# Optimization experiments

Hardware: AMD Instinct MI355X
Metric: run time of the kernel (lower is better)

The kernel has to match this reference:

```python
import jax, jax.numpy as jnp
import numpy as np

B, L, E, H = 8, 2048, 1024, 16
D = E // H
EPS = 1e-6


def setup_inputs() -> dict:
    key = jax.random.key(0)
    ks = jax.random.split(key, 9)
    s = 1.0 / np.sqrt(E)
    def lin_w(k):
        return jax.random.uniform(k, (E, E), jnp.float32, -s, s)
    def lin_b(k):
        return jax.random.uniform(k, (E,), jnp.float32, -s, s)
    return {
        "query": jax.random.normal(ks[0], (B, L, E), jnp.float32),
        "Wq": lin_w(ks[1]), "bq": lin_b(ks[2]),
        "Wk": lin_w(ks[3]), "bk": lin_b(ks[4]),
        "Wv": lin_w(ks[5]), "bv": lin_b(ks[6]),
        "Wo": lin_w(ks[7]), "bo": lin_b(ks[8]),
    }


def reference(query, Wq, bq, Wk, bk, Wv, bv, Wo, bo):
    bsz, tgt_len, embed_dim = query.shape
    n_head = H
    head_dim = embed_dim // n_head
    m = tgt_len  # src_len == tgt_len (self-attention)

    # projections (torch Linear with W stored as (in, out) here)
    q = query @ Wq + bq
    k = query @ Wk + bk
    v = query @ Wv + bv

    # (B, L, E) -> (B, H, L, D), softmax feature map over head dim
    def to_heads(x):
        return x.reshape(bsz, tgt_len, n_head, head_dim).transpose(0, 2, 1, 3)

    q = jax.nn.softmax(to_heads(q), axis=-1)
    k = jax.nn.softmax(to_heads(k), axis=-1)
    v = to_heads(v)
    comp_q = 1.0 - q
    comp_k = 1.0 - k

    # cosFormer positional reweighting: idx = (pi/2) * (1..m) / m
    idx = (np.pi / 2) * jnp.arange(1, m + 1, dtype=jnp.float32) / m  # (L,)
    sin = jnp.sin(idx)[None, None, :, None]  # (1,1,L,1)
    cos = jnp.cos(idx)[None, None, :, None]

    def feat(x):  # (B,H,L,D) -> (B,H,L,2D)
        return jnp.concatenate([x * sin, x * cos], axis=-1)

    qf, comp_qf = feat(q), feat(comp_q)
    kf, comp_kf = feat(k), feat(comp_k)

    def branch(qf_, kf_):
        kv = jnp.einsum('bhld,bhlm->bhdm', kf_, v)            # (B,H,2D,D)
        z = 1.0 / jnp.maximum(
            jnp.einsum('bhld,bhd->bhl', qf_, kf_.sum(axis=2)), EPS)
        return jnp.einsum('bhld,bhdm,bhl->bhlm', qf_, kv, z)  # (B,H,L,D)

    attn = branch(qf, kf) + branch(comp_qf, comp_kf)

    # torch: (B*H,L,D).transpose(0,1).view(L,B,E)
    out = attn.transpose(2, 0, 1, 3).reshape(tgt_len, bsz, embed_dim)
    out = out @ Wo + bo
    # torch final: .view(bsz, tgt_len, n_feat) -- raw reshape, no transpose
    return out.reshape(bsz, tgt_len, embed_dim)
```

## Files before the change

kernel.cpp:

```cpp
#include <hip/hip_runtime.h>
#include <hip/hip_bf16.h>
#include <cstdint>

#define B_   8
#define L_   2048
#define E_   1024
#define H_   16
#define D_   64
#define M_   (B_ * L_)
#define EPS_ 1e-6f
#define PI2_ 1.57079632679f

typedef __bf16 bf16;
typedef __bf16 bf16x8 __attribute__((ext_vector_type(8)));
typedef __bf16 bf16x4 __attribute__((ext_vector_type(4)));
typedef float  floatx4 __attribute__((ext_vector_type(4)));

__device__ inline void async_cp16(const void* g, void* l) {
  __builtin_amdgcn_global_load_lds(
      (__attribute__((address_space(1))) void*)const_cast<void*>(g),
      (__attribute__((address_space(3))) void*)l,
      16, 0, 0);
}

__global__ __launch_bounds__(256) void k_convert_x(const float* __restrict__ x,
                                                   bf16* __restrict__ o) {
  size_t i = ((size_t)blockIdx.x * 256 + threadIdx.x) * 8;
  floatx4 a = *(const floatx4*)(x + i);
  floatx4 b = *(const floatx4*)(x + i + 4);
  bf16x8 r;
  r[0] = (bf16)a[0]; r[1] = (bf16)a[1]; r[2] = (bf16)a[2]; r[3] = (bf16)a[3];
  r[4] = (bf16)b[0]; r[5] = (bf16)b[1]; r[6] = (bf16)b[2]; r[7] = (bf16)b[3];
  *(bf16x8*)(o + i) = r;
}

struct TArgs { const float* src[4]; bf16* dst[4]; };

__global__ __launch_bounds__(256) void k_transpose_w(TArgs t) {
  __shared__ float tile[32][33];
  const float* src = t.src[blockIdx.z];
  bf16* dst = t.dst[blockIdx.z];
  int bx = blockIdx.x, by = blockIdx.y;
  int x = threadIdx.x, y = threadIdx.y;
#pragma unroll
  for (int i = 0; i < 4; i++) {
    int r = by * 32 + y + i * 8;
    tile[y + i * 8][x] = src[(size_t)r * E_ + bx * 32 + x];
  }
  __syncthreads();
#pragma unroll
  for (int i = 0; i < 4; i++) {
    int r = bx * 32 + y + i * 8;
    dst[(size_t)r * E_ + by * 32 + x] = (bf16)tile[x][y + i * 8];
  }
}

#define BAR()   asm volatile("s_barrier" ::: "memory")
#define LGKM0() asm volatile("s_waitcnt lgkmcnt(0)" ::: "memory")
#define VMW4()  asm volatile("s_waitcnt vmcnt(4)" ::: "memory")
#define VMW0()  asm volatile("s_waitcnt vmcnt(0)" ::: "memory")
#define MFMA_   __builtin_amdgcn_mfma_f32_16x16x32_bf16

#define GEMM_TILE(t_, c_) {                                                    \
    const int t = (t_); const int c = (c_);                                    \
    bf16x8 a0[4][2], a1[4][2], b0[2][2], b1[2][2];                             \
                                                                  \
    _Pragma("unroll") for (int i = 0; i < 4; i++) {                            \
      a0[i][0] = RDA(c, 0, i); a0[i][1] = RDA(c, 1, i); }                      \
    _Pragma("unroll") for (int j = 0; j < 2; j++) {                            \
      b0[j][0] = RDB(c, 0, j); b0[j][1] = RDB(c, 1, j); }                      \
    if (t + 1 < 16) STAGE(c ^ 1, 0, t + 1, 0);                                 \
    BAR(); LGKM0();                                                            \
    __builtin_amdgcn_s_setprio(1);                                             \
    _Pragma("unroll") for (int i = 0; i < 4; i++)                              \
      _Pragma("unroll") for (int j = 0; j < 2; j++) {                          \
        acc[i][j] = MFMA_(a0[i][0], b0[j][0], acc[i][j], 0, 0, 0);             \
        acc[i][j] = MFMA_(a0[i][1], b0[j][1], acc[i][j], 0, 0, 0); }           \
    __builtin_amdgcn_s_setprio(0);                                             \
    BAR();                                                                     \
                                                                  \
    _Pragma("unroll") for (int j = 0; j < 2; j++) {                            \
      b1[j][0] = RDB(c, 0, j + 2); b1[j][1] = RDB(c, 1, j + 2); }              \
    if (t + 1 < 16) STAGE(c ^ 1, 0, t + 1, 1);                                 \
    BAR(); LGKM0();                                                            \
    __builtin_amdgcn_s_setprio(1);                                             \
    _Pragma("unroll") for (int i = 0; i < 4; i++)                              \
      _Pragma("unroll") for (int j = 0; j < 2; j++) {                          \
        acc[i][j + 2] = MFMA_(a0[i][0], b1[j][0], acc[i][j + 2], 0, 0, 0);     \
        acc[i][j + 2] = MFMA_(a0[i][1], b1[j][1], acc[i][j + 2], 0, 0, 0); }   \
    __builtin_amdgcn_s_setprio(0);                                             \
    BAR();                                                                     \
                                                                  \
    _Pragma("unroll") for (int i = 0; i < 4; i++) {                            \
      a1[i][0] = RDA(c, 0, i + 4); a1[i][1] = RDA(c, 1, i + 4); }              \
    if (t + 2 < 16) STAGE(c, 1, t + 2, 0);                                     \
    BAR(); LGKM0();                                                            \
    __builtin_amdgcn_s_setprio(1);                                             \
    _Pragma("unroll") for (int i = 0; i < 4; i++)                              \
      _Pragma("unroll") for (int j = 0; j < 2; j++) {                          \
        acc[i + 4][j + 2] = MFMA_(a1[i][0], b1[j][0], acc[i + 4][j + 2], 0, 0, 0); \
        acc[i + 4][j + 2] = MFMA_(a1[i][1], b1[j][1], acc[i + 4][j + 2], 0, 0, 0); } \
    __builtin_amdgcn_s_setprio(0);                                             \
    BAR();                                                                     \
                                                                  \
    if (t < 14) { STAGE(c, 1, t + 2, 1); VMW4(); } else { VMW0(); }            \
    BAR();                                                                     \
    __builtin_amdgcn_s_setprio(1);                                             \
    _Pragma("unroll") for (int i = 0; i < 4; i++)                              \
      _Pragma("unroll") for (int j = 0; j < 2; j++) {                          \
        acc[i + 4][j] = MFMA_(a1[i][0], b0[j][0], acc[i + 4][j], 0, 0, 0);     \
        acc[i + 4][j] = MFMA_(a1[i][1], b0[j][1], acc[i + 4][j], 0, 0, 0); }   \
    __builtin_amdgcn_s_setprio(0);                                             \
    BAR();                                                                     \
  }

__device__ __forceinline__ void gemm256_core(const bf16* __restrict__ Agl,
                                             const bf16* __restrict__ Bgl,
                                             int bm, int bn, bf16* ldsb,
                                             floatx4 (&acc)[8][4]) {
  const int tid  = threadIdx.x;
  const int wid  = tid >> 6;
  const int lane = tid & 63;
  const int quad = lane >> 4;
  const int l15  = lane & 15;
  const int wm   = wid >> 2;
  const int wn   = wid & 3;
  const int rb   = wn * 32;
  const int gcol = wm * 32 + (((lane & 3) * 8) ^ ((lane & 32) ? 16 : 0));
  const bf16* pA = Agl + (size_t)(bm * 256 + rb + (lane >> 2)) * E_ + gcol;
  const bf16* pB = Bgl + (size_t)(bn * 256 + rb + (lane >> 2)) * E_ + gcol;
  const int aCol = (quad * 8) ^ ((l15 & 8) ? 16 : 0);

  auto LDSP = [&](int c, int mat, int qq, int row, int col) -> bf16* {
    return ldsb + ((((c * 2 + mat) * 2 + qq) * 256 + row) * 32 + col);
  };
  auto STAGE = [&](int c, int mat, int tt, int h) {
    const bf16* g = (mat ? pB : pA) + (size_t)(h * 128) * E_ + tt * 64;
    bf16* lp = LDSP(c, mat, wm, h * 128 + rb, 0);
    async_cp16(g, lp);
    async_cp16(g + (size_t)16 * E_, lp + 16 * 32);
  };
  auto RDA = [&](int c, int qq, int i) -> bf16x8 {
    return *(const bf16x8*)LDSP(c, 0, qq, wm * 128 + i * 16 + l15, aCol);
  };
  auto RDB = [&](int c, int qq, int j) -> bf16x8 {
    return *(const bf16x8*)LDSP(c, 1, qq, wn * 64 + j * 16 + l15, aCol);
  };

  STAGE(0, 1, 0, 0); STAGE(0, 1, 0, 1);
  STAGE(0, 0, 0, 0); STAGE(0, 0, 0, 1);
  STAGE(1, 1, 1, 0); STAGE(1, 1, 1, 1);
  VMW4();
  BAR();

#pragma unroll 1
  for (int tb = 0; tb < 16; tb += 2) {
    GEMM_TILE(tb, 0)
    GEMM_TILE(tb + 1, 1)
  }
}

__global__ __launch_bounds__(512, 2) void k_gemm_qkv256(
    const bf16* __restrict__ A, const bf16* __restrict__ Wt,
    const float* __restrict__ bq, const float* __restrict__ bk,
    const float* __restrict__ bv,
    bf16* __restrict__ QTb, bf16* __restrict__ KTb, bf16* __restrict__ VT) {
  __shared__ __attribute__((aligned(16))) bf16 ldsb[2 * 2 * 2 * 256 * 32];
  const int id  = blockIdx.x;
  const int xcd = id & 7, rr = id >> 3;
  const int bm  = xcd * 8 + rr / 12;
  const int cz  = rr % 12;
  const int bn  = cz & 3, z = cz >> 2;
  const bf16* Bgl = Wt + (size_t)z * E_ * E_;

  floatx4 acc[8][4] = {};
  gemm256_core(A, Bgl, bm, bn, ldsb, acc);

  const int tid  = threadIdx.x;
  const int wid  = tid >> 6;
  const int lane = tid & 63;
  const int quad = lane >> 4;
  const int l15  = lane & 15;
  const int wm   = wid >> 2, wn = wid & 3;
  const float* bias = (z == 0) ? bq : (z == 1) ? bk : bv;
  float bb[4];
#pragma unroll
  for (int j = 0; j < 4; j++) bb[j] = bias[bn * 256 + wn * 64 + j * 16 + l15];

  if (z < 2) {
#pragma unroll
    for (int i = 0; i < 8; i++)
#pragma unroll
      for (int r = 0; r < 4; r++) {
        float v0 = acc[i][0][r] + bb[0];
        float v1 = acc[i][1][r] + bb[1];
        float v2 = acc[i][2][r] + bb[2];
        float v3 = acc[i][3][r] + bb[3];
        float m = fmaxf(fmaxf(v0, v1), fmaxf(v2, v3));
        m = fmaxf(m, __shfl_xor(m, 1));
        m = fmaxf(m, __shfl_xor(m, 2));
        m = fmaxf(m, __shfl_xor(m, 4));
        m = fmaxf(m, __shfl_xor(m, 8));
        v0 = __expf(v0 - m); v1 = __expf(v1 - m);
        v2 = __expf(v2 - m); v3 = __expf(v3 - m);
        float s = v0 + v1 + v2 + v3;
        s += __shfl_xor(s, 1); s += __shfl_xor(s, 2);
        s += __shfl_xor(s, 4); s += __shfl_xor(s, 8);
        const float inv = 1.f / s;
        acc[i][0][r] = v0 * inv; acc[i][1][r] = v1 * inv;
        acc[i][2][r] = v2 * inv; acc[i][3][r] = v3 * inv;
      }
  } else {
#pragma unroll
    for (int i = 0; i < 8; i++)
#pragma unroll
      for (int j = 0; j < 4; j++) {
        acc[i][j][0] += bb[j]; acc[i][j][1] += bb[j];
        acc[i][j][2] += bb[j]; acc[i][j][3] += bb[j];
      }
  }

  bf16* OT = (z == 0) ? QTb : (z == 1) ? KTb : VT;
#pragma unroll
  for (int i = 0; i < 8; i++)
#pragma unroll
    for (int j = 0; j < 4; j++) {
      const int c  = bn * 256 + wn * 64 + j * 16 + l15;
      const int r0 = bm * 256 + wm * 128 + i * 16 + quad * 4;
      const int h = c >> 6, d = c & 63;
      const int b = r0 >> 11, l = r0 & 2047;
      bf16x4 rv;
      rv[0] = (bf16)acc[i][j][0]; rv[1] = (bf16)acc[i][j][1];
      rv[2] = (bf16)acc[i][j][2]; rv[3] = (bf16)acc[i][j][3];
      *(bf16x4*)&OT[(((size_t)(b * 16 + h) * 64 + d) * 2048) + l] = rv;
    }
}

__global__ __launch_bounds__(512, 2) void k_gemm_final256(
    const bf16* __restrict__ A, const bf16* __restrict__ Bt,
    const float* __restrict__ bias, float* __restrict__ C) {
  __shared__ __attribute__((aligned(16))) bf16 ldsb[2 * 2 * 2 * 256 * 32];
  const int id  = blockIdx.x;
  const int xcd = id & 7, rr = id >> 3;
  const int bm  = xcd * 8 + (rr >> 2);
  const int bn  = rr & 3;

  floatx4 acc[8][4] = {};
  gemm256_core(A, Bt, bm, bn, ldsb, acc);

  const int tid  = threadIdx.x;
  const int wid  = tid >> 6;
  const int lane = tid & 63;
  const int quad = lane >> 4;
  const int l15  = lane & 15;
  const int wm   = wid >> 2, wn = wid & 3;
#pragma unroll
  for (int i = 0; i < 8; i++)
#pragma unroll
    for (int j = 0; j < 4; j++) {
      const int col = bn * 256 + wn * 64 + j * 16 + l15;
      const float bb = bias[col];
#pragma unroll
      for (int r = 0; r < 4; r++) {
        const int row = bm * 256 + wm * 128 + i * 16 + quad * 4 + r;
        C[(size_t)row * E_ + col] = acc[i][j][r] + bb;
      }
    }
}

__global__ __launch_bounds__(256) void k_kv(const bf16* __restrict__ KTb,
                                            const bf16* __restrict__ VT,
                                            float* __restrict__ kvp) {
  __shared__ __attribute__((aligned(16))) bf16 ktb[64 * 32];
  __shared__ __attribute__((aligned(16))) bf16 vt[64 * 32];
  __shared__ __attribute__((aligned(16))) bf16 Bsn[64 * 40];
  __shared__ __attribute__((aligned(16))) bf16 Bcs[64 * 40];
  __shared__ float snl[32], csl[32];
  const int kseg = blockIdx.x;
  const int bh   = blockIdx.y;
  const int t = threadIdx.x;
  const int wid = t >> 6, lane = t & 63;
  const int quad = lane >> 4, l15 = lane & 15;
  const int wm = wid >> 1, wn = wid & 1;

  const bf16* ktg = KTb + (size_t)bh * 64 * 2048;
  const bf16* vtg = VT  + (size_t)bh * 64 * 2048;

  floatx4 acc[4][2] = {};
  float rs = 0.f;
  const int d_ = t & 63, h_ = t >> 6;

  for (int it = 0; it < 16; it++) {
    const int l0 = kseg * 512 + it * 32;
    {
      const int r = lane >> 2, ch = lane & 3;
      const bf16* gk = ktg + (size_t)(wid * 16 + r) * 2048 + l0 + ((ch ^ (r & 1)) * 8);
      async_cp16(gk, &ktb[(wid * 16) * 32]);
      const bf16* gv = vtg + (size_t)(wid * 16 + r) * 2048 + l0 + ch * 8;
      async_cp16(gv, &vt[(wid * 16) * 32]);
    }
    if (t < 32) {
      const float ang = PI2_ * (float)(l0 + t + 1) / (float)L_;
      snl[t] = __sinf(ang); csl[t] = __cosf(ang);
    }
    __syncthreads();

    {
      const int row = t >> 2, cc = (t & 3) * 8;
      bf16x8 v = *(const bf16x8*)&vt[row * 32 + cc];
      bf16x8 a, b;
#pragma unroll
      for (int e = 0; e < 8; e++) {
        const float f = (float)v[e];
        a[e] = (bf16)(f * snl[cc + e]);
        b[e] = (bf16)(f * csl[cc + e]);
      }
      *(bf16x8*)&Bsn[row * 40 + cc] = a;
      *(bf16x8*)&Bcs[row * 40 + cc] = b;
    }
    if (t < 128) {
      float r8 = 0.f;
#pragma unroll
      for (int p = 0; p < 4; p++) {
        bf16x8 v = *(const bf16x8*)&ktb[d_ * 32 + p * 8];
        const int gl = (p ^ (d_ & 1)) * 8;
#pragma unroll
        for (int e = 0; e < 8; e++)
          r8 += (float)v[e] * (h_ ? csl[gl + e] : snl[gl + e]);
      }
      rs += r8;
    }
    __syncthreads();

    bf16x8 af[4], bfm[2];
    const bf16* Bsel = wm ? Bcs : Bsn;
#pragma unroll
    for (int i = 0; i < 4; i++)
      af[i] = *(const bf16x8*)&ktb[(i * 16 + l15) * 32 + ((quad ^ (l15 & 1)) * 8)];
#pragma unroll
    for (int j = 0; j < 2; j++)
      bfm[j] = *(const bf16x8*)&Bsel[(wn * 32 + j * 16 + l15) * 40 + quad * 8];
#pragma unroll
    for (int i = 0; i < 4; i++)
#pragma unroll
      for (int j = 0; j < 2; j++)
        acc[i][j] = __builtin_amdgcn_mfma_f32_16x16x32_bf16(af[i], bfm[j], acc[i][j], 0, 0, 0);
    __syncthreads();
  }

  float* C = kvp + (size_t)(kseg * 128 + bh) * 128 * 68;
#pragma unroll
  for (int i = 0; i < 4; i++)
#pragma unroll
    for (int j = 0; j < 2; j++) {
      const int col = wn * 32 + j * 16 + l15;
#pragma unroll
      for (int r = 0; r < 4; r++) {
        const int row = wm * 64 + i * 16 + quad * 4 + r;
        C[(size_t)row * 68 + col] = acc[i][j][r];
      }
    }
  if (t < 128) C[(size_t)t * 68 + 64] = rs;
}

__global__ __launch_bounds__(64) void k_consts(const float* __restrict__ kvp,
                                               bf16* __restrict__ KVT,
                                               float* __restrict__ ksbuf) {
  const int bh = blockIdx.x;
  const int dp = threadIdx.x;
  const size_t gs = (size_t)128 * 128 * 68;
  const float* P = kvp + (size_t)bh * 128 * 68;
  bf16* kr = KVT + (size_t)(bh * 64 + dp) * 160;
  float sk0 = 0.f, sk1 = 0.f;
#pragma unroll 8
  for (int f = 0; f < 128; f++) {
    float v = P[(size_t)f * 68 + dp] + P[gs + (size_t)f * 68 + dp]
            + P[2 * gs + (size_t)f * 68 + dp] + P[3 * gs + (size_t)f * 68 + dp];
    kr[f] = (bf16)v;
    if (f < 64) sk0 += v; else sk1 += v;
  }
  float ks0 = P[(size_t)dp * 68 + 64] + P[gs + (size_t)dp * 68 + 64]
            + P[2 * gs + (size_t)dp * 68 + 64] + P[3 * gs + (size_t)dp * 68 + 64];
  float ks1 = P[(size_t)(64 + dp) * 68 + 64] + P[gs + (size_t)(64 + dp) * 68 + 64]
            + P[2 * gs + (size_t)(64 + dp) * 68 + 64] + P[3 * gs + (size_t)(64 + dp) * 68 + 64];
  ksbuf[(size_t)bh * 136 + dp]      = ks0;
  ksbuf[(size_t)bh * 136 + 64 + dp] = ks1;
  float sks0 = ks0, sks1 = ks1;
#pragma unroll
  for (int o = 1; o < 64; o <<= 1) { sks0 += __shfl_xor(sks0, o); sks1 += __shfl_xor(sks1, o); }
  kr[128] = (bf16)(62.f * sk0);
  kr[129] = (bf16)(62.f * sk1);
#pragma unroll
  for (int f = 130; f < 160; f++) kr[f] = (bf16)0.f;
  if (dp == 0) {
    ksbuf[(size_t)bh * 136 + 128] = sks0;
    ksbuf[(size_t)bh * 136 + 129] = sks1;
  }
}

#define ASTR 168
__global__ __launch_bounds__(256) void k_attn(const bf16* __restrict__ QTb,
                                              const bf16* __restrict__ KVT,
                                              const float* __restrict__ ksbuf,
                                              bf16* __restrict__ attn) {
  __shared__ __attribute__((aligned(16))) bf16 Abuf[128 * ASTR];
  __shared__ __attribute__((aligned(16))) bf16 Bbuf[64 * ASTR];
  __shared__ float ksl[136];
  const int lc = blockIdx.x;
  const int bh = blockIdx.y;
  const int b = bh >> 4, h = bh & 15;
  const int t = threadIdx.x;

  {
    const bf16* src = KVT + (size_t)bh * 64 * 160;
#pragma unroll
    for (int i = 0; i < 5; i++) {
      const int idx = t + i * 256;
      const int row = idx / 20, ch = idx % 20;
      *(bf16x8*)&Bbuf[row * ASTR + ch * 8] = *(const bf16x8*)(src + row * 160 + ch * 8);
    }
    if (t < 130) ksl[t] = ksbuf[(size_t)bh * 136 + t];
  }
  __syncthreads();

  if (t < 128) {
    const int l = lc * 128 + t;
    const bf16* qp = QTb + (size_t)bh * 64 * 2048 + l;
    float xv[64];
#pragma unroll
    for (int d = 0; d < 64; d++) xv[d] = (float)qp[(size_t)d * 2048];
    float t0 = 0.f, t1 = 0.f;
#pragma unroll
    for (int d = 0; d < 64; d++) {
      t0 += xv[d] * ksl[d];
      t1 += xv[d] * ksl[64 + d];
    }
    const float SKS0 = ksl[128], SKS1 = ksl[129];
    const float ang = PI2_ * (float)(l + 1) / (float)L_;
    const float sn = __sinf(ang), cs = __cosf(ang);
    const float den1 = sn * t0 + cs * t1;
    const float den2 = sn * (62.f * SKS0 + t0) + cs * (62.f * SKS1 + t1);
    const float z1 = 1.f / fmaxf(den1, EPS_);
    const float z2 = 1.f / fmaxf(den2, EPS_);
    const float zz = z1 + z2;
    const float a0 = zz * sn, a1 = zz * cs;
    bf16* ar = &Abuf[t * ASTR];
#pragma unroll
    for (int g = 0; g < 8; g++) {
      bf16x8 w;
#pragma unroll
      for (int j = 0; j < 8; j++) w[j] = (bf16)(a0 * xv[g * 8 + j]);
      *(bf16x8*)(ar + g * 8) = w;
    }
#pragma unroll
    for (int g = 0; g < 8; g++) {
      bf16x8 w;
#pragma unroll
      for (int j = 0; j < 8; j++) w[j] = (bf16)(a1 * xv[g * 8 + j]);
      *(bf16x8*)(ar + 64 + g * 8) = w;
    }
    bf16x8 wt = {};
    wt[0] = (bf16)(z2 * sn); wt[1] = (bf16)(z2 * cs);
    *(bf16x8*)(ar + 128) = wt;
    bf16x8 zr = {};
    *(bf16x8*)(ar + 136) = zr;
    *(bf16x8*)(ar + 144) = zr;
    *(bf16x8*)(ar + 152) = zr;
  }
  __syncthreads();

  const int wid = t >> 6, lane = t & 63;
  const int quad = lane >> 4, l15 = lane & 15;
  const int wm = wid >> 1, wn = wid & 1;
  floatx4 acc[4][2] = {};
#pragma unroll
  for (int kk = 0; kk < 5; kk++) {
    bf16x8 af[4], bfm[2];
#pragma unroll
    for (int i = 0; i < 4; i++)
      af[i] = *(const bf16x8*)&Abuf[(wm * 64 + i * 16 + l15) * ASTR + kk * 32 + quad * 8];
#pragma unroll
    for (int j = 0; j < 2; j++)
      bfm[j] = *(const bf16x8*)&Bbuf[(wn * 32 + j * 16 + l15) * ASTR + kk * 32 + quad * 8];
#pragma unroll
    for (int i = 0; i < 4; i++)
#pragma unroll
      for (int j = 0; j < 2; j++)
        acc[i][j] = __builtin_amdgcn_mfma_f32_16x16x32_bf16(af[i], bfm[j], acc[i][j], 0, 0, 0);
  }
#pragma unroll
  for (int i = 0; i < 4; i++)
#pragma unroll
    for (int j = 0; j < 2; j++) {
      const int dp = wn * 32 + j * 16 + l15;
#pragma unroll
      for (int r = 0; r < 4; r++) {
        const int l = lc * 128 + wm * 64 + i * 16 + quad * 4 + r;
        attn[((size_t)l * B_ + b) * E_ + h * 64 + dp] = (bf16)acc[i][j][r];
      }
    }
}

extern "C" void kernel_launch(void* const* d_in, const int* in_sizes, int n_in,
                              void* d_out, int out_size, void* d_ws, size_t ws_size,
                              hipStream_t stream) {
  (void)in_sizes; (void)n_in; (void)out_size; (void)ws_size;
  const float* query = (const float*)d_in[0];
  const float* Wq = (const float*)d_in[1];
  const float* bq = (const float*)d_in[2];
  const float* Wk = (const float*)d_in[3];
  const float* bk = (const float*)d_in[4];
  const float* Wv = (const float*)d_in[5];
  const float* bv = (const float*)d_in[6];
  const float* Wo = (const float*)d_in[7];
  const float* bo = (const float*)d_in[8];

  char* ws = (char*)d_ws;
  bf16*  QTb  = (bf16*) (ws + 0);
  bf16*  KTb  = (bf16*) (ws + 33554432);
  bf16*  VT   = (bf16*) (ws + 67108864);
  bf16*  Wt   = (bf16*) (ws + 100663296);
  bf16*  Xbf  = (bf16*) (ws + 109051904);
  bf16*  attnb= (bf16*) (ws + 109051904);
  float* kvp  = (float*)(ws + 142606336);
  bf16*  KVT  = (bf16*) (ws + 160432128);
  float* ksbuf= (float*)(ws + 163053568);

  k_convert_x<<<(M_ * E_) / (256 * 8), 256, 0, stream>>>(query, Xbf);

  TArgs ta;
  ta.src[0] = Wq; ta.src[1] = Wk; ta.src[2] = Wv; ta.src[3] = Wo;
  ta.dst[0] = Wt;                       ta.dst[1] = Wt + (size_t)E_ * E_;
  ta.dst[2] = Wt + (size_t)2 * E_ * E_; ta.dst[3] = Wt + (size_t)3 * E_ * E_;
  k_transpose_w<<<dim3(32, 32, 4), dim3(32, 8), 0, stream>>>(ta);

  k_gemm_qkv256<<<768, 512, 0, stream>>>(Xbf, Wt, bq, bk, bv, QTb, KTb, VT);

  k_kv<<<dim3(4, 128), 256, 0, stream>>>(KTb, VT, kvp);

  k_consts<<<128, 64, 0, stream>>>(kvp, KVT, ksbuf);

  k_attn<<<dim3(16, 128), 256, 0, stream>>>(QTb, KVT, ksbuf, attnb);

  k_gemm_final256<<<256, 512, 0, stream>>>(attnb, Wt + (size_t)3 * E_ * E_, bo, (float*)d_out);
}
```

Baseline: 374.3 us.

## Stage QKV epilogue through LDS for coalesced stores; widen consts and attn prologue

```diff
diff --git a/kernel.cpp b/kernel.cpp
--- a/kernel.cpp
+++ b/kernel.cpp
@@ -177,8 +177,8 @@
   gemm256_core(A, Bgl, bm, bn, ldsb, acc);
 
   const int tid  = threadIdx.x;
+  const int lane = tid & 63;
   const int wid  = tid >> 6;
-  const int lane = tid & 63;
   const int quad = lane >> 4;
   const int l15  = lane & 15;
   const int wm   = wid >> 2, wn = wid & 3;
@@ -220,20 +220,31 @@
       }
   }
 
-  bf16* OT = (z == 0) ? QTb : (z == 1) ? KTb : VT;
+  bf16* rep = ldsb;
 #pragma unroll
   for (int i = 0; i < 8; i++)
 #pragma unroll
     for (int j = 0; j < 4; j++) {
-      const int c  = bn * 256 + wn * 64 + j * 16 + l15;
-      const int r0 = bm * 256 + wm * 128 + i * 16 + quad * 4;
-      const int h = c >> 6, d = c & 63;
-      const int b = r0 >> 11, l = r0 & 2047;
+      const int c    = wn * 64 + j * 16 + l15;
+      const int lrow = wm * 128 + i * 16 + quad * 4;
       bf16x4 rv;
       rv[0] = (bf16)acc[i][j][0]; rv[1] = (bf16)acc[i][j][1];
       rv[2] = (bf16)acc[i][j][2]; rv[3] = (bf16)acc[i][j][3];
-      *(bf16x4*)&OT[(((size_t)(b * 16 + h) * 64 + d) * 2048) + l] = rv;
-    }
+      *(bf16x4*)&rep[(c * 256 + lrow) ^ ((c & 7) << 3)] = rv;
+    }
+  __syncthreads();
+
+  bf16* OT = (z == 0) ? QTb : (z == 1) ? KTb : VT;
+  const int b  = bm >> 3;
+  const int lb = (bm & 7) * 256;
+#pragma unroll
+  for (int k = 0; k < 16; k++) {
+    const int c   = k * 16 + (tid >> 5);
+    const int lch = tid & 31;
+    const int cg  = bn * 256 + c;
+    bf16x8 v = *(const bf16x8*)&rep[(c * 256 + lch * 8) ^ ((c & 7) << 3)];
+    *(bf16x8*)&OT[((size_t)((b * 16 + (cg >> 6)) * 64 + (cg & 63))) * 2048 + lb + lch * 8] = v;
+  }
 }
 
 __global__ __launch_bounds__(512, 2) void k_gemm_final256(
@@ -363,38 +374,49 @@
   if (t < 128) C[(size_t)t * 68 + 64] = rs;
 }
 
-__global__ __launch_bounds__(64) void k_consts(const float* __restrict__ kvp,
-                                               bf16* __restrict__ KVT,
-                                               float* __restrict__ ksbuf) {
+__global__ __launch_bounds__(256) void k_consts(const float* __restrict__ kvp,
+                                                bf16* __restrict__ KVT,
+                                                float* __restrict__ ksbuf) {
+  __shared__ float red[4][64];
+  __shared__ float sksh[2];
   const int bh = blockIdx.x;
-  const int dp = threadIdx.x;
+  const int t  = threadIdx.x;
+  const int fq = t >> 6, dp = t & 63;
   const size_t gs = (size_t)128 * 128 * 68;
   const float* P = kvp + (size_t)bh * 128 * 68;
   bf16* kr = KVT + (size_t)(bh * 64 + dp) * 160;
-  float sk0 = 0.f, sk1 = 0.f;
+  float sp = 0.f;
 #pragma unroll 8
-  for (int f = 0; f < 128; f++) {
+  for (int f = fq * 32; f < fq * 32 + 32; f++) {
     float v = P[(size_t)f * 68 + dp] + P[gs + (size_t)f * 68 + dp]
             + P[2 * gs + (size_t)f * 68 + dp] + P[3 * gs + (size_t)f * 68 + dp];
     kr[f] = (bf16)v;
-    if (f < 64) sk0 += v; else sk1 += v;
-  }
-  float ks0 = P[(size_t)dp * 68 + 64] + P[gs + (size_t)dp * 68 + 64]
-            + P[2 * gs + (size_t)dp * 68 + 64] + P[3 * gs + (size_t)dp * 68 + 64];
-  float ks1 = P[(size_t)(64 + dp) * 68 + 64] + P[gs + (size_t)(64 + dp) * 68 + 64]
-            + P[2 * gs + (size_t)(64 + dp) * 68 + 64] + P[3 * gs + (size_t)(64 + dp) * 68 + 64];
-  ksbuf[(size_t)bh * 136 + dp]      = ks0;
-  ksbuf[(size_t)bh * 136 + 64 + dp] = ks1;
-  float sks0 = ks0, sks1 = ks1;
-#pragma unroll
-  for (int o = 1; o < 64; o <<= 1) { sks0 += __shfl_xor(sks0, o); sks1 += __shfl_xor(sks1, o); }
-  kr[128] = (bf16)(62.f * sk0);
-  kr[129] = (bf16)(62.f * sk1);
-#pragma unroll
-  for (int f = 130; f < 160; f++) kr[f] = (bf16)0.f;
-  if (dp == 0) {
-    ksbuf[(size_t)bh * 136 + 128] = sks0;
-    ksbuf[(size_t)bh * 136 + 129] = sks1;
+    sp += v;
+  }
+  red[fq][dp] = sp;
+  float ksv = 0.f;
+  if (t < 128) {
+    ksv = P[(size_t)t * 68 + 64] + P[gs + (size_t)t * 68 + 64]
+        + P[2 * gs + (size_t)t * 68 + 64] + P[3 * gs + (size_t)t * 68 + 64];
+    ksbuf[(size_t)bh * 136 + t] = ksv;
+  }
+  float sks = ksv;
+#pragma unroll
+  for (int o = 1; o < 64; o <<= 1) sks += __shfl_xor(sks, o);
+  if (t == 0)  sksh[0] = sks;
+  if (t == 64) sksh[1] = sks;
+  __syncthreads();
+  if (t < 64) {
+    const float sk0 = red[0][t] + red[1][t];
+    const float sk1 = red[2][t] + red[3][t];
+    kr[128] = (bf16)(62.f * sk0);
+    kr[129] = (bf16)(62.f * sk1);
+#pragma unroll
+    for (int f = 130; f < 160; f++) kr[f] = (bf16)0.f;
+    if (t == 0) {
+      ksbuf[(size_t)bh * 136 + 128] = sksh[0];
+      ksbuf[(size_t)bh * 136 + 129] = sksh[1];
+    }
   }
 }
 
@@ -406,6 +428,7 @@
   __shared__ __attribute__((aligned(16))) bf16 Abuf[128 * ASTR];
   __shared__ __attribute__((aligned(16))) bf16 Bbuf[64 * ASTR];
   __shared__ float ksl[136];
+  __shared__ float pth0[2][128], pth1[2][128];
   const int lc = blockIdx.x;
   const int bh = blockIdx.y;
   const int b = bh >> 4, h = bh & 15;
@@ -423,18 +446,26 @@
   }
   __syncthreads();
 
-  if (t < 128) {
-    const int l = lc * 128 + t;
-    const bf16* qp = QTb + (size_t)bh * 64 * 2048 + l;
-    float xv[64];
-#pragma unroll
-    for (int d = 0; d < 64; d++) xv[d] = (float)qp[(size_t)d * 2048];
-    float t0 = 0.f, t1 = 0.f;
-#pragma unroll
-    for (int d = 0; d < 64; d++) {
-      t0 += xv[d] * ksl[d];
-      t1 += xv[d] * ksl[64 + d];
-    }
+  const int lr = t & 127, hf = t >> 7;
+  const int l  = lc * 128 + lr;
+  float xv[32];
+  {
+    const bf16* qp = QTb + (size_t)bh * 64 * 2048 + (size_t)(hf * 32) * 2048 + l;
+#pragma unroll
+    for (int d = 0; d < 32; d++) xv[d] = (float)qp[(size_t)d * 2048];
+    float pa = 0.f, pb = 0.f;
+#pragma unroll
+    for (int d = 0; d < 32; d++) {
+      pa += xv[d] * ksl[hf * 32 + d];
+      pb += xv[d] * ksl[64 + hf * 32 + d];
+    }
+    pth0[hf][lr] = pa; pth1[hf][lr] = pb;
+  }
+  __syncthreads();
+
+  {
+    const float t0 = pth0[0][lr] + pth0[1][lr];
+    const float t1 = pth1[0][lr] + pth1[1][lr];
     const float SKS0 = ksl[128], SKS1 = ksl[129];
     const float ang = PI2_ * (float)(l + 1) / (float)L_;
     const float sn = __sinf(ang), cs = __cosf(ang);
@@ -444,28 +475,30 @@
     const float z2 = 1.f / fmaxf(den2, EPS_);
     const float zz = z1 + z2;
     const float a0 = zz * sn, a1 = zz * cs;
-    bf16* ar = &Abuf[t * ASTR];
-#pragma unroll
-    for (int g = 0; g < 8; g++) {
+    bf16* ar = &Abuf[lr * ASTR];
+#pragma unroll
+    for (int g = 0; g < 4; g++) {
       bf16x8 w;
 #pragma unroll
       for (int j = 0; j < 8; j++) w[j] = (bf16)(a0 * xv[g * 8 + j]);
-      *(bf16x8*)(ar + g * 8) = w;
-    }
-#pragma unroll
-    for (int g = 0; g < 8; g++) {
+      *(bf16x8*)(ar + hf * 32 + g * 8) = w;
+    }
+#pragma unroll
+    for (int g = 0; g < 4; g++) {
       bf16x8 w;
 #pragma unroll
       for (int j = 0; j < 8; j++) w[j] = (bf16)(a1 * xv[g * 8 + j]);
-      *(bf16x8*)(ar + 64 + g * 8) = w;
-    }
-    bf16x8 wt = {};
-    wt[0] = (bf16)(z2 * sn); wt[1] = (bf16)(z2 * cs);
-    *(bf16x8*)(ar + 128) = wt;
-    bf16x8 zr = {};
-    *(bf16x8*)(ar + 136) = zr;
-    *(bf16x8*)(ar + 144) = zr;
-    *(bf16x8*)(ar + 152) = zr;
+      *(bf16x8*)(ar + 64 + hf * 32 + g * 8) = w;
+    }
+    if (hf) {
+      bf16x8 wt = {};
+      wt[0] = (bf16)(z2 * sn); wt[1] = (bf16)(z2 * cs);
+      *(bf16x8*)(ar + 128) = wt;
+      bf16x8 zr = {};
+      *(bf16x8*)(ar + 136) = zr;
+      *(bf16x8*)(ar + 144) = zr;
+      *(bf16x8*)(ar + 152) = zr;
+    }
   }
   __syncthreads();
 
@@ -495,8 +528,8 @@
       const int dp = wn * 32 + j * 16 + l15;
 #pragma unroll
       for (int r = 0; r < 4; r++) {
-        const int l = lc * 128 + wm * 64 + i * 16 + quad * 4 + r;
-        attn[((size_t)l * B_ + b) * E_ + h * 64 + dp] = (bf16)acc[i][j][r];
+        const int lo = lc * 128 + wm * 64 + i * 16 + quad * 4 + r;
+        attn[((size_t)lo * B_ + b) * E_ + h * 64 + dp] = (bf16)acc[i][j][r];
       }
     }
 }
@@ -538,7 +571,7 @@
 
   k_kv<<<dim3(4, 128), 256, 0, stream>>>(KTb, VT, kvp);
 
-  k_consts<<<128, 64, 0, stream>>>(kvp, KVT, ksbuf);
+  k_consts<<<128, 256, 0, stream>>>(kvp, KVT, ksbuf);
 
   k_attn<<<dim3(16, 128), 256, 0, stream>>>(QTb, KVT, ksbuf, attnb);
 
```

After: 351.1 us. 1.07x faster.
